# Performance work log

Measured on AMD Instinct MI355X. Metric: run time of the kernel, lower is better.

## Reference

```python
import jax, jax.numpy as jnp
import numpy as np

SEQ, BATCH, IN, HID, OUT = 2048, 1, 2048, 4096, 2048


def setup_inputs() -> dict:
    key = jax.random.key(0)
    ks = jax.random.split(key, 5)
    s_ih = 1.0 / np.sqrt(IN + HID)
    inp = {
        "input": jax.random.normal(ks[0], (SEQ, BATCH, IN), dtype=jnp.float32),
        "W_i2h": jax.random.uniform(ks[1], (HID, IN + HID), minval=-s_ih, maxval=s_ih, dtype=jnp.float32),
        "b_i2h": jax.random.uniform(ks[2], (HID,), minval=-s_ih, maxval=s_ih, dtype=jnp.float32),
        "W_i2o": jax.random.uniform(ks[3], (OUT, IN + HID), minval=-s_ih, maxval=s_ih, dtype=jnp.float32),
        "b_i2o": jax.random.uniform(ks[4], (OUT,), minval=-s_ih, maxval=s_ih, dtype=jnp.float32),
    }
    return inp


def reference(input, W_i2h, b_i2h, W_i2o, b_i2o):
    # input: [S, 1, IN]; hidden: [1, HID]
    h0 = jnp.zeros((BATCH, HID), dtype=input.dtype)

    def step(h, x):
        combined = jnp.concatenate([x, h], axis=1)  # [1, IN+HID]
        h_new = jax.nn.sigmoid(combined @ W_i2h.T + b_i2h)  # [1, HID]
        out = combined @ W_i2o.T + b_i2o                    # [1, OUT]
        return h_new, out

    _, outs = jax.lax.scan(step, h0, input)
    return outs[-1]  # module returns output of the last timestep
```

## Files before the change

### kernel.cpp

```cpp
#include <hip/hip_runtime.h>
#include <hip/hip_bf16.h>
#include <stdint.h>

#define SEQ 2048
#define IN_DIM 2048
#define HID 4096
#define CONCAT 6144
#define OUT_DIM 2048

typedef __attribute__((ext_vector_type(8))) short s8v;
typedef __attribute__((ext_vector_type(4))) float f4v;

#define SENT 0xFFFFFFFFu
#define SPIN_BUDGET 20000


__global__ __launch_bounds__(256) void k1_prep(const float* __restrict__ X,
                                               const float* __restrict__ Wi2h,
                                               __hip_bfloat16* __restrict__ Xb,
                                               __hip_bfloat16* __restrict__ Wxb) {
  int gid = blockIdx.x * blockDim.x + threadIdx.x;
  int stride = gridDim.x * blockDim.x;
  for (int i = gid; i < SEQ * IN_DIM; i += stride)
    Xb[i] = __float2bfloat16(X[i]);
  for (int i = gid; i < HID * IN_DIM; i += stride) {
    int r = i >> 11, c = i & (IN_DIM - 1);
    Wxb[i] = __float2bfloat16(Wi2h[(long long)r * CONCAT + c]);
  }
}

__global__ __launch_bounds__(256) void k2_zgemm(const __hip_bfloat16* __restrict__ Xb,
                                                const __hip_bfloat16* __restrict__ Wxb,
                                                const float* __restrict__ bias,
                                                float* __restrict__ Z) {
  __shared__ __align__(16) __hip_bfloat16 As[64][40];
  __shared__ __align__(16) __hip_bfloat16 Bs[64][40];
  const int bm = blockIdx.x & 31;
  const int bn = blockIdx.x >> 5;
  const int tid = threadIdx.x;
  const int wv = tid >> 6, l = tid & 63;
  const int wr = (wv >> 1) * 32, wc = (wv & 1) * 32;
  const int fr = l & 15, fko = (l >> 4) * 8;

  f4v acc[2][2] = {};
  const int r = tid >> 2, cc = (tid & 3) * 8;
  const __hip_bfloat16* ga = Xb + (long long)(bm * 64 + r) * IN_DIM + cc;
  const __hip_bfloat16* gb = Wxb + (long long)(bn * 64 + r) * IN_DIM + cc;

  for (int k0 = 0; k0 < IN_DIM; k0 += 32) {
    *(s8v*)&As[r][cc] = *(const s8v*)(ga + k0);
    *(s8v*)&Bs[r][cc] = *(const s8v*)(gb + k0);
    __syncthreads();
    s8v a0 = *(const s8v*)&As[wr + fr][fko];
    s8v a1 = *(const s8v*)&As[wr + 16 + fr][fko];
    s8v b0 = *(const s8v*)&Bs[wc + fr][fko];
    s8v b1 = *(const s8v*)&Bs[wc + 16 + fr][fko];
    acc[0][0] = __builtin_amdgcn_mfma_f32_16x16x32_bf16(a0, b0, acc[0][0], 0, 0, 0);
    acc[0][1] = __builtin_amdgcn_mfma_f32_16x16x32_bf16(a0, b1, acc[0][1], 0, 0, 0);
    acc[1][0] = __builtin_amdgcn_mfma_f32_16x16x32_bf16(a1, b0, acc[1][0], 0, 0, 0);
    acc[1][1] = __builtin_amdgcn_mfma_f32_16x16x32_bf16(a1, b1, acc[1][1], 0, 0, 0);
    __syncthreads();
  }
#pragma unroll
  for (int fm = 0; fm < 2; ++fm)
#pragma unroll
    for (int fn = 0; fn < 2; ++fn)
#pragma unroll
      for (int i = 0; i < 4; ++i) {
        int row = bm * 64 + wr + fm * 16 + (l >> 4) * 4 + i;
        int col = bn * 64 + wc + fn * 16 + fr;
        Z[(long long)row * HID + col] = acc[fm][fn][i] + bias[col];
      }
}

__global__ __launch_bounds__(512, 1) void k3_rnn(const float* __restrict__ Wi2h,
                                                 const float* __restrict__ Z,
                                                 float* __restrict__ hbuf) {
  const int w = blockIdx.x;
  const int tid = threadIdx.x;
  const int v = tid >> 6;
  const int l = tid & 63;
  const int rowbase = w * 16;
  const int kbase = v * 512 + l;

  float Wreg[16][8];
#pragma unroll
  for (int r = 0; r < 16; ++r) {
    const float* src = Wi2h + (long long)(rowbase + r) * CONCAT + IN_DIM + kbase;
#pragma unroll
    for (int j = 0; j < 8; ++j) Wreg[r][j] = src[64 * j];
  }
#pragma unroll
  for (int r = 0; r < 16; ++r)
#pragma unroll
    for (int j = 0; j < 8; ++j)
      asm volatile("" : "+v"(Wreg[r][j]));

  __shared__ float part[2][8][16];
  const int lm = l & 15;
  const int r_mine = ((lm & 1) << 3) | ((lm & 2) << 1) | ((lm & 4) >> 1) | ((lm & 8) >> 3);

  for (int t = 0; t < SEQ - 1; ++t) {
    float zv = 0.f;
    if (v == 0 && l < 16) zv = Z[(long long)t * HID + rowbase + l];

    float acc[16];
#pragma unroll
    for (int r = 0; r < 16; ++r) acc[r] = 0.f;

    if (t > 0) {
      const uint32_t* hrow = (const uint32_t*)hbuf + (long long)t * HID + kbase;
      bool done[8];
#pragma unroll
      for (int j = 0; j < 8; ++j) done[j] = false;
      int spins = 0;
      while (true) {
        uint32_t uj[8];
#pragma unroll
        for (int j = 0; j < 8; ++j)
          if (!done[j])
            uj[j] = __hip_atomic_load(hrow + 64 * j, __ATOMIC_RELAXED, __HIP_MEMORY_SCOPE_AGENT);
        bool alldone = true;
#pragma unroll
        for (int j = 0; j < 8; ++j) {
          if (!done[j]) {
            if (__all(uj[j] != SENT)) {
              float h = __builtin_bit_cast(float, uj[j]);
#pragma unroll
              for (int r = 0; r < 16; ++r)
                acc[r] = fmaf(Wreg[r][j], h, acc[r]);
              done[j] = true;
            } else {
              alldone = false;
            }
          }
        }
        if (alldone) break;
        if (++spins > SPIN_BUDGET) break;
      }
    }

#pragma unroll
    for (int i = 0; i < 8; ++i) {
      float send = (l & 1) ? acc[i] : acc[i + 8];
      float keep = (l & 1) ? acc[i + 8] : acc[i];
      acc[i] = keep + __shfl_xor(send, 1, 64);
    }
#pragma unroll
    for (int i = 0; i < 4; ++i) {
      float send = (l & 2) ? acc[i] : acc[i + 4];
      float keep = (l & 2) ? acc[i + 4] : acc[i];
      acc[i] = keep + __shfl_xor(send, 2, 64);
    }
#pragma unroll
    for (int i = 0; i < 2; ++i) {
      float send = (l & 4) ? acc[i] : acc[i + 2];
      float keep = (l & 4) ? acc[i + 2] : acc[i];
      acc[i] = keep + __shfl_xor(send, 4, 64);
    }
    {
      float send = (l & 8) ? acc[0] : acc[1];
      float keep = (l & 8) ? acc[1] : acc[0];
      acc[0] = keep + __shfl_xor(send, 8, 64);
    }
    float rsum = acc[0];
    rsum += __shfl_xor(rsum, 16, 64);
    rsum += __shfl_xor(rsum, 32, 64);

    const int b = t & 1;
    if (l < 16) part[b][v][r_mine] = rsum;
    __syncthreads();

    if (v == 0 && l < 16) {
      float s = 0.f;
#pragma unroll
      for (int q = 0; q < 8; ++q) s += part[b][q][l];
      float pre = s + zv;
      float hn = 1.0f / (1.0f + __expf(-pre));
      __hip_atomic_store(hbuf + (long long)(t + 1) * HID + rowbase + l, hn,
                         __ATOMIC_RELAXED, __HIP_MEMORY_SCOPE_AGENT);
    }
  }
}

__global__ __launch_bounds__(256) void k4_out(const float* __restrict__ X,
                                              const float* __restrict__ Wi2o,
                                              const float* __restrict__ bi2o,
                                              const float* __restrict__ hbuf,
                                              float* __restrict__ out) {
  const int v = threadIdx.x >> 6, l = threadIdx.x & 63;
  const int o = blockIdx.x * 4 + v;
  const float* wrow = Wi2o + (long long)o * CONCAT;
  const float* xlast = X + (long long)(SEQ - 1) * IN_DIM;
  const float* hlast = hbuf + (long long)(SEQ - 1) * HID;
  float s = 0.f;
  for (int k = l; k < IN_DIM; k += 64) s = fmaf(wrow[k], xlast[k], s);
  for (int k = l; k < HID; k += 64) s = fmaf(wrow[IN_DIM + k], hlast[k], s);
#pragma unroll
  for (int m = 1; m < 64; m <<= 1) s += __shfl_xor(s, m, 64);
  if (l == 0) out[o] = s + bi2o[o];
}

extern "C" void kernel_launch(void* const* d_in, const int* in_sizes, int n_in,
                              void* d_out, int out_size, void* d_ws, size_t ws_size,
                              hipStream_t stream) {
  (void)in_sizes; (void)n_in; (void)out_size; (void)ws_size;
  const float* X    = (const float*)d_in[0];
  const float* Wi2h = (const float*)d_in[1];
  const float* bi2h = (const float*)d_in[2];
  const float* Wi2o = (const float*)d_in[3];
  const float* bi2o = (const float*)d_in[4];
  float* out = (float*)d_out;

  char* ws = (char*)d_ws;
  float* Z            = (float*)(ws);
  float* hbuf         = (float*)(ws + 33554432);
  __hip_bfloat16* Xb  = (__hip_bfloat16*)(ws + 33554432);
  __hip_bfloat16* Wxb = (__hip_bfloat16*)(ws + 41943040);

  hipLaunchKernelGGL(k1_prep, dim3(2048), dim3(256), 0, stream, X, Wi2h, Xb, Wxb);
  hipLaunchKernelGGL(k2_zgemm, dim3(2048), dim3(256), 0, stream, Xb, Wxb, bi2h, Z);

  hipMemsetAsync(hbuf, 0xFF, 33554432, stream);

  void* args[] = { (void*)&Wi2h, (void*)&Z, (void*)&hbuf };
  hipLaunchCooperativeKernel((void*)k3_rnn, dim3(256), dim3(512), args, 0, stream);

  hipLaunchKernelGGL(k4_out, dim3(512), dim3(256), 0, stream, X, Wi2o, bi2o, hbuf, out);
}
```

Before: 5.620 ms.

## Poll hidden state via async global-to-LDS loads with triple-buffered rotation

Replaces the per-step spin on atomic global loads of the previous hidden state with global_load_lds issues rotated across three LDS buffers, so several poll requests are in flight and each is checked as it lands. A bounded rotation is followed by a fallback atomic-load spin. The Z prefetch also moves to an async LDS load, and the final cross-wave reduction is spread across all eight waves using shuffles instead of a single wave summing serially. The intent is to cut latency on the sequential critical path of the recurrence. In exchange it adds manual waitcnt and barrier handling, with the risk of stale LDS reads or extra memory traffic from polling.

```diff
diff --git a/kernel.cpp b/kernel.cpp
--- a/kernel.cpp
+++ b/kernel.cpp
@@ -12,7 +12,8 @@
 typedef __attribute__((ext_vector_type(4))) float f4v;
 
 #define SENT 0xFFFFFFFFu
-#define SPIN_BUDGET 20000
+#define ROT_BUDGET 150
+#define FB_BUDGET 20000
 
 
 __global__ __launch_bounds__(256) void k1_prep(const float* __restrict__ X,
@@ -96,48 +97,84 @@
     for (int j = 0; j < 8; ++j)
       asm volatile("" : "+v"(Wreg[r][j]));
 
-  __shared__ float part[2][8][16];
+  __shared__ uint32_t pbuf[3][8][8][64];
+  __shared__ float zbuf[8][64];
+  __shared__ float part[2][8][17];
   const int lm = l & 15;
   const int r_mine = ((lm & 1) << 3) | ((lm & 2) << 1) | ((lm & 4) >> 1) | ((lm & 8) >> 3);
 
+#define FMAG(uu, dd, jj)                                                          \
+  if (!dd && __all((uu) != SENT)) {                                               \
+    float h_ = __builtin_bit_cast(float, (uu));                                   \
+    _Pragma("unroll")                                                             \
+    for (int r = 0; r < 16; ++r) acc[r] = fmaf(Wreg[r][jj], h_, acc[r]);          \
+    dd = true;                                                                    \
+  }
+
+#define GISSUE(RB)                                                                \
+  _Pragma("unroll")                                                               \
+  for (int j = 0; j < 8; ++j)                                                     \
+    __builtin_amdgcn_global_load_lds(hsrc + 64 * j, &pbuf[RB][v][j][0], 4, 0, 17);
+
+#define POLLCHK(RB)                                                               \
+  asm volatile("s_waitcnt vmcnt(16)" ::: "memory");                               \
+  __builtin_amdgcn_sched_barrier(0);                                              \
+  {                                                                               \
+    uint32_t u_;                                                                  \
+    u_ = pbuf[RB][v][0][l]; FMAG(u_, d0, 0)                                       \
+    u_ = pbuf[RB][v][1][l]; FMAG(u_, d1, 1)                                       \
+    u_ = pbuf[RB][v][2][l]; FMAG(u_, d2, 2)                                       \
+    u_ = pbuf[RB][v][3][l]; FMAG(u_, d3, 3)                                       \
+    u_ = pbuf[RB][v][4][l]; FMAG(u_, d4, 4)                                       \
+    u_ = pbuf[RB][v][5][l]; FMAG(u_, d5, 5)                                       \
+    u_ = pbuf[RB][v][6][l]; FMAG(u_, d6, 6)                                       \
+    u_ = pbuf[RB][v][7][l]; FMAG(u_, d7, 7)                                       \
+  }
+
+#define ALLD (d0 && d1 && d2 && d3 && d4 && d5 && d6 && d7)
+
+#pragma clang loop unroll(disable)
   for (int t = 0; t < SEQ - 1; ++t) {
-    float zv = 0.f;
-    if (v == 0 && l < 16) zv = Z[(long long)t * HID + rowbase + l];
+    const float* zsrc = Z + (long long)t * HID + rowbase + 2 * v + (l & 1);
+    __builtin_amdgcn_global_load_lds(zsrc, &zbuf[v][0], 4, 0, 0);
 
     float acc[16];
 #pragma unroll
     for (int r = 0; r < 16; ++r) acc[r] = 0.f;
+    bool d0 = false, d1 = false, d2 = false, d3 = false,
+         d4 = false, d5 = false, d6 = false, d7 = false;
 
     if (t > 0) {
-      const uint32_t* hrow = (const uint32_t*)hbuf + (long long)t * HID + kbase;
-      bool done[8];
-#pragma unroll
-      for (int j = 0; j < 8; ++j) done[j] = false;
-      int spins = 0;
-      while (true) {
-        uint32_t uj[8];
-#pragma unroll
-        for (int j = 0; j < 8; ++j)
-          if (!done[j])
-            uj[j] = __hip_atomic_load(hrow + 64 * j, __ATOMIC_RELAXED, __HIP_MEMORY_SCOPE_AGENT);
-        bool alldone = true;
-#pragma unroll
-        for (int j = 0; j < 8; ++j) {
-          if (!done[j]) {
-            if (__all(uj[j] != SENT)) {
-              float h = __builtin_bit_cast(float, uj[j]);
-#pragma unroll
-              for (int r = 0; r < 16; ++r)
-                acc[r] = fmaf(Wreg[r][j], h, acc[r]);
-              done[j] = true;
-            } else {
-              alldone = false;
-            }
-          }
+      const uint32_t* hsrc = (const uint32_t*)hbuf + (long long)t * HID + kbase;
+      GISSUE(0) GISSUE(1) GISSUE(2)
+      int rot = 0;
+      for (;;) {
+        POLLCHK(0) if (ALLD) break;
+        GISSUE(0)
+        POLLCHK(1) if (ALLD) break;
+        GISSUE(1)
+        POLLCHK(2) if (ALLD) break;
+        GISSUE(2)
+        if (++rot > ROT_BUDGET) break;
+      }
+      if (!ALLD) {
+        int spins = 0;
+        for (;;) {
+          uint32_t u_;
+          if (!d0) { u_ = __hip_atomic_load(hsrc + 0,   __ATOMIC_RELAXED, __HIP_MEMORY_SCOPE_AGENT); FMAG(u_, d0, 0) }
+          if (!d1) { u_ = __hip_atomic_load(hsrc + 64,  __ATOMIC_RELAXED, __HIP_MEMORY_SCOPE_AGENT); FMAG(u_, d1, 1) }
+          if (!d2) { u_ = __hip_atomic_load(hsrc + 128, __ATOMIC_RELAXED, __HIP_MEMORY_SCOPE_AGENT); FMAG(u_, d2, 2) }
+          if (!d3) { u_ = __hip_atomic_load(hsrc + 192, __ATOMIC_RELAXED, __HIP_MEMORY_SCOPE_AGENT); FMAG(u_, d3, 3) }
+          if (!d4) { u_ = __hip_atomic_load(hsrc + 256, __ATOMIC_RELAXED, __HIP_MEMORY_SCOPE_AGENT); FMAG(u_, d4, 4) }
+          if (!d5) { u_ = __hip_atomic_load(hsrc + 320, __ATOMIC_RELAXED, __HIP_MEMORY_SCOPE_AGENT); FMAG(u_, d5, 5) }
+          if (!d6) { u_ = __hip_atomic_load(hsrc + 384, __ATOMIC_RELAXED, __HIP_MEMORY_SCOPE_AGENT); FMAG(u_, d6, 6) }
+          if (!d7) { u_ = __hip_atomic_load(hsrc + 448, __ATOMIC_RELAXED, __HIP_MEMORY_SCOPE_AGENT); FMAG(u_, d7, 7) }
+          if (ALLD) break;
+          if (++spins > FB_BUDGET) break;
         }
-        if (alldone) break;
-        if (++spins > SPIN_BUDGET) break;
-      }
+      }
+    } else {
+      asm volatile("s_waitcnt vmcnt(0)" ::: "memory");
     }
 
 #pragma unroll
@@ -167,20 +204,28 @@
     rsum += __shfl_xor(rsum, 16, 64);
     rsum += __shfl_xor(rsum, 32, 64);
 
-    const int b = t & 1;
-    if (l < 16) part[b][v][r_mine] = rsum;
-    __syncthreads();
-
-    if (v == 0 && l < 16) {
-      float s = 0.f;
-#pragma unroll
-      for (int q = 0; q < 8; ++q) s += part[b][q][l];
-      float pre = s + zv;
-      float hn = 1.0f / (1.0f + __expf(-pre));
-      __hip_atomic_store(hbuf + (long long)(t + 1) * HID + rowbase + l, hn,
-                         __ATOMIC_RELAXED, __HIP_MEMORY_SCOPE_AGENT);
-    }
-  }
+    const int bb = t & 1;
+    if (l < 16) part[bb][v][r_mine] = rsum;
+    asm volatile("s_waitcnt lgkmcnt(0)" ::: "memory");
+    __builtin_amdgcn_s_barrier();
+
+    {
+      float p = part[bb][(l >> 1) & 7][2 * v + (l & 1)];
+      p += __shfl_xor(p, 2, 64);
+      p += __shfl_xor(p, 4, 64);
+      p += __shfl_xor(p, 8, 64);
+      if (l < 2) {
+        float pre = p + zbuf[v][l];
+        float hn = 1.0f / (1.0f + __expf(-pre));
+        __hip_atomic_store(hbuf + (long long)(t + 1) * HID + rowbase + 2 * v + l, hn,
+                           __ATOMIC_RELAXED, __HIP_MEMORY_SCOPE_AGENT);
+      }
+    }
+  }
+#undef FMAG
+#undef GISSUE
+#undef POLLCHK
+#undef ALLD
 }
 
 __global__ __launch_bounds__(256) void k4_out(const float* __restrict__ X,
```

New measurement: 10.73 ms. 1.91x slower.
